# Performance work log

Measured on AMD Instinct MI355X. Metric: run time of the kernel, lower is better.

Reference implementation:

```python
import jax, jax.numpy as jnp
import numpy as np

N_NODES = 50000
N_EDGES = 800000
LATENT = 32
NODE_IN = 6
EDGE_IN = 3
STEPS = 10
OUT_DIM = 1
NEG_SLOPE = 0.01
LN_EPS = 1e-5


def _leaky(x):
    return jnp.where(x >= 0, x, NEG_SLOPE * x)


def _layernorm(x, scale, bias):
    mu = jnp.mean(x, axis=-1, keepdims=True)
    var = jnp.mean(jnp.square(x - mu), axis=-1, keepdims=True)
    return (x - mu) * jax.lax.rsqrt(var + LN_EPS) * scale + bias


def setup_inputs() -> dict:
    key = jax.random.key(0)
    ks = jax.random.split(key, 24)
    g = lambda i, shape, fan_in: (jax.random.normal(ks[i], shape, jnp.float32)
                                  / np.sqrt(fan_in)).astype(jnp.float32)
    return {
        "x": jax.random.normal(ks[0], (N_NODES, NODE_IN), jnp.float32),
        "edge_attr": jax.random.normal(ks[1], (N_EDGES, EDGE_IN), jnp.float32),
        "senders": jax.random.randint(ks[2], (N_EDGES,), 0, N_NODES, jnp.int32),
        "receivers": jax.random.randint(ks[3], (N_EDGES,), 0, N_NODES, jnp.int32),
        # input embedders (Linear + LeakyReLU)
        "node_enc_W": g(4, (NODE_IN, LATENT), NODE_IN),
        "node_enc_b": jnp.zeros((LATENT,), jnp.float32),
        "edge_enc_W": g(5, (EDGE_IN, LATENT), EDGE_IN),
        "edge_enc_b": jnp.zeros((LATENT,), jnp.float32),
        # per-step edge update: concat(e, x_src, x_dst) -> latent
        "edge_W": g(6, (STEPS, 3 * LATENT, LATENT), 3 * LATENT),
        "edge_b": jnp.zeros((STEPS, LATENT), jnp.float32),
        "edge_ln_scale": jnp.ones((STEPS, LATENT), jnp.float32),
        "edge_ln_bias": jnp.zeros((STEPS, LATENT), jnp.float32),
        # per-step node update: concat(x, agg) -> latent
        "node_W": g(7, (STEPS, 2 * LATENT, LATENT), 2 * LATENT),
        "node_b": jnp.zeros((STEPS, LATENT), jnp.float32),
        "node_ln_scale": jnp.ones((STEPS, LATENT), jnp.float32),
        "node_ln_bias": jnp.zeros((STEPS, LATENT), jnp.float32),
        # decoder
        "dec_W1": g(8, (LATENT, LATENT), LATENT),
        "dec_b1": jnp.zeros((LATENT,), jnp.float32),
        "dec_W2": g(9, (LATENT, OUT_DIM), LATENT),
        "dec_b2": jnp.zeros((OUT_DIM,), jnp.float32),
    }


def _forward(x, edge_attr, senders, receivers,
             node_enc_W, node_enc_b, edge_enc_W, edge_enc_b,
             edge_W, edge_b, edge_ln_scale, edge_ln_bias,
             node_W, node_b, node_ln_scale, node_ln_bias,
             dec_W1, dec_b1, dec_W2, dec_b2):
    n = x.shape[0]
    # encode raw features into latent space
    h = _leaky(x @ node_enc_W + node_enc_b)            # [N, L]
    e = _leaky(edge_attr @ edge_enc_W + edge_enc_b)    # [E, L]
    # receiver in-degree for scatter-mean (constant across steps)
    cnt = jax.ops.segment_sum(jnp.ones((e.shape[0],), e.dtype), receivers,
                              num_segments=n)
    inv_cnt = (1.0 / jnp.maximum(cnt, 1.0))[:, None]   # [N, 1]

    def step(carry, p):
        h, e = carry
        eW, eb, es, ebi, nW, nb, ns, nbi = p
        # edge update: MLP(concat(e, h_src, h_dst)) + inner LN + residual
        m = jnp.concatenate([e, h[senders], h[receivers]], axis=-1)  # [E, 3L]
        m = _layernorm(_leaky(m @ eW + eb), es, ebi)
        e = e + m
        # node update: scatter-mean over receivers, MLP + inner LN + residual
        agg = jax.ops.segment_sum(e, receivers, num_segments=n) * inv_cnt
        u = jnp.concatenate([h, agg], axis=-1)                       # [N, 2L]
        u = _layernorm(_leaky(u @ nW + nb), ns, nbi)
        h = h + u
        return (h, e), None

    (h, e), _ = jax.lax.scan(step, (h, e),
                             (edge_W, edge_b, edge_ln_scale, edge_ln_bias,
                              node_W, node_b, node_ln_scale, node_ln_bias))
    # decoder: Linear -> LeakyReLU -> Linear
    return _leaky(h @ dec_W1 + dec_b1) @ dec_W2 + dec_b2  # [N, 1]


def reference(x, edge_attr, senders, receivers,
              node_enc_W, node_enc_b, edge_enc_W, edge_enc_b,
              edge_W, edge_b, edge_ln_scale, edge_ln_bias,
              node_W, node_b, node_ln_scale, node_ln_bias,
              dec_W1, dec_b1, dec_W2, dec_b2):
    return _forward(x, edge_attr, senders, receivers,
                    node_enc_W, node_enc_b, edge_enc_W, edge_enc_b,
                    edge_W, edge_b, edge_ln_scale, edge_ln_bias,
                    node_W, node_b, node_ln_scale, node_ln_bias,
                    dec_W1, dec_b1, dec_W2, dec_b2)
```

## Files before the change

kernel.cpp:

```cpp
#include <hip/hip_runtime.h>
#include <hip/hip_bf16.h>

#define N_NODES 50000
#define N_EDGES 800000
#define LATENT 32
#define STEPS 10
#define NEG_SLOPE 0.01f
#define LN_EPS 1e-5f
#define SCAN_BLK 256
#define SCAN_NBLK ((N_NODES + SCAN_BLK - 1) / SCAN_BLK)
#define STG_STRIDE 36
#define NODES_PER_BLOCK 32
#define STEP_BLOCKS ((N_NODES + NODES_PER_BLOCK - 1) / NODES_PER_BLOCK)
#define WS_STRIDE 36

typedef __attribute__((ext_vector_type(8))) __bf16 bf16x8;
typedef __attribute__((ext_vector_type(4))) __bf16 bf16x4;
typedef __attribute__((ext_vector_type(4))) float f32x4;

__device__ __forceinline__ float leaky(float x) {
    return x >= 0.0f ? x : NEG_SLOPE * x;
}

__device__ __forceinline__ float4 f4fma(float a, float4 b, float4 c) {
    c.x += a * b.x; c.y += a * b.y; c.z += a * b.z; c.w += a * b.w;
    return c;
}

__device__ __forceinline__ bf16x4 pack4(float4 v) {
    bf16x4 o;
    o[0] = (__bf16)v.x; o[1] = (__bf16)v.y; o[2] = (__bf16)v.z; o[3] = (__bf16)v.w;
    return o;
}


__global__ void encode_nodes_kernel(const float* __restrict__ x,
                                    const float* __restrict__ W,
                                    const float* __restrict__ b,
                                    float* __restrict__ h,
                                    __bf16* __restrict__ hbf) {
    __shared__ __align__(16) float Ws[6 * 32];
    __shared__ __align__(16) float bs[32];
    int tid = threadIdx.x;
    if (tid < 192) Ws[tid] = W[tid];
    if (tid < 32) bs[tid] = b[tid];
    __syncthreads();
    int n = blockIdx.x * blockDim.x + tid;
    if (n >= N_NODES) return;
    float xv[6];
#pragma unroll
    for (int k = 0; k < 6; k++) xv[k] = x[(size_t)n * 6 + k];
    float4 acc[8];
#pragma unroll
    for (int q = 0; q < 8; q++) acc[q] = *(const float4*)&bs[q * 4];
#pragma unroll
    for (int k = 0; k < 6; k++) {
#pragma unroll
        for (int q = 0; q < 8; q++) {
            float4 w = *(const float4*)&Ws[k * 32 + q * 4];
            acc[q] = f4fma(xv[k], w, acc[q]);
        }
    }
#pragma unroll
    for (int q = 0; q < 8; q++) {
        float4 o = acc[q];
        o.x = leaky(o.x); o.y = leaky(o.y); o.z = leaky(o.z); o.w = leaky(o.w);
        *(float4*)&h[(size_t)n * 32 + q * 4] = o;
        *(bf16x4*)&hbf[(size_t)n * 32 + q * 4] = pack4(o);
    }
}


__global__ void count_kernel(const int* __restrict__ recv, int* __restrict__ cnt) {
    int i = blockIdx.x * blockDim.x + threadIdx.x;
    if (i < N_EDGES) atomicAdd(&cnt[recv[i]], 1);
}

__global__ void csr_reduce_kernel(const int* __restrict__ cnt, int* __restrict__ partial) {
    __shared__ int sdata[SCAN_BLK];
    int tid = threadIdx.x;
    int idx = blockIdx.x * SCAN_BLK + tid;
    sdata[tid] = (idx < N_NODES) ? cnt[idx] : 0;
    __syncthreads();
#pragma unroll
    for (int off = SCAN_BLK / 2; off > 0; off >>= 1) {
        if (tid < off) sdata[tid] += sdata[tid + off];
        __syncthreads();
    }
    if (tid == 0) partial[blockIdx.x] = sdata[0];
}

__global__ void csr_scan_partials_kernel(int* __restrict__ partial,
                                         int* __restrict__ row_start) {
    __shared__ int sdata[SCAN_BLK];
    int tid = threadIdx.x;
    int v = (tid < SCAN_NBLK) ? partial[tid] : 0;
    sdata[tid] = v;
    __syncthreads();
#pragma unroll
    for (int off = 1; off < SCAN_BLK; off <<= 1) {
        int t = (tid >= off) ? sdata[tid - off] : 0;
        __syncthreads();
        sdata[tid] += t;
        __syncthreads();
    }
    if (tid < SCAN_NBLK) partial[tid] = sdata[tid] - v;
    if (tid == SCAN_BLK - 1) row_start[N_NODES] = sdata[SCAN_BLK - 1];
}

__global__ void csr_apply_kernel(const int* __restrict__ cnt,
                                 const int* __restrict__ partial,
                                 int* __restrict__ row_start,
                                 int* __restrict__ cursor) {
    __shared__ int sdata[SCAN_BLK];
    int tid = threadIdx.x;
    int idx = blockIdx.x * SCAN_BLK + tid;
    int v = (idx < N_NODES) ? cnt[idx] : 0;
    sdata[tid] = v;
    __syncthreads();
#pragma unroll
    for (int off = 1; off < SCAN_BLK; off <<= 1) {
        int t = (tid >= off) ? sdata[tid - off] : 0;
        __syncthreads();
        sdata[tid] += t;
        __syncthreads();
    }
    if (idx < N_NODES) {
        int out = partial[blockIdx.x] + sdata[tid] - v;
        row_start[idx] = out;
        cursor[idx] = out;
    }
}

__global__ void scatter_encode_kernel(const float* __restrict__ ea,
                                      const int* __restrict__ senders,
                                      const int* __restrict__ receivers,
                                      int* __restrict__ cursor,
                                      const float* __restrict__ W,
                                      const float* __restrict__ b,
                                      __bf16* __restrict__ e,
                                      unsigned int* __restrict__ sr_p) {
    __shared__ __align__(16) float Ws[3 * 32];
    __shared__ __align__(16) float bs[32];
    int tid = threadIdx.x;
    if (tid < 96) Ws[tid] = W[tid];
    if (tid < 32) bs[tid] = b[tid];
    __syncthreads();
    int i = blockIdx.x * blockDim.x + tid;
    if (i >= N_EDGES) return;
    int s = senders[i];
    int r = receivers[i];
    float xv[3];
#pragma unroll
    for (int k = 0; k < 3; k++) xv[k] = ea[(size_t)i * 3 + k];
    int pos = atomicAdd(&cursor[r], 1);
    float4 acc[8];
#pragma unroll
    for (int q = 0; q < 8; q++) acc[q] = *(const float4*)&bs[q * 4];
#pragma unroll
    for (int k = 0; k < 3; k++) {
#pragma unroll
        for (int q = 0; q < 8; q++) {
            float4 w = *(const float4*)&Ws[k * 32 + q * 4];
            acc[q] = f4fma(xv[k], w, acc[q]);
        }
    }
    __bf16* er = e + (size_t)pos * 32;
#pragma unroll
    for (int q = 0; q < 4; q++) {
        float4 lo = acc[2 * q], hi = acc[2 * q + 1];
        bf16x8 v;
        v[0] = (__bf16)leaky(lo.x); v[1] = (__bf16)leaky(lo.y);
        v[2] = (__bf16)leaky(lo.z); v[3] = (__bf16)leaky(lo.w);
        v[4] = (__bf16)leaky(hi.x); v[5] = (__bf16)leaky(hi.y);
        v[6] = (__bf16)leaky(hi.z); v[7] = (__bf16)leaky(hi.w);
        *(bf16x8*)(er + q * 8) = v;
    }
    sr_p[pos] = (unsigned int)s | ((unsigned int)r << 16);
}


__global__ __launch_bounds__(256) void fused_step_kernel(
    __bf16* __restrict__ e,
    const __bf16* __restrict__ hbf_in,
    __bf16* __restrict__ hbf_out,
    const float* __restrict__ h_in,
    float* __restrict__ h_out,
    const unsigned int* __restrict__ srp,
    const int* __restrict__ row_start,
    const float* __restrict__ eW,
    const float* __restrict__ eb,
    const float* __restrict__ els,
    const float* __restrict__ elb,
    const float* __restrict__ nW,
    const float* __restrict__ nb,
    const float* __restrict__ nls,
    const float* __restrict__ nlb) {
    __shared__ __align__(16) float stg[4][16 * STG_STRIDE];
    __shared__ __align__(16) float Ws[64 * WS_STRIDE];
    __shared__ __align__(16) float prm[96];

    int tid = threadIdx.x;
    const int wave = tid >> 6;
    const int lane = tid & 63;
    const int n_ = lane & 15;
    const int quad = lane >> 4;
    const int rr = lane >> 2;
    const int jj = lane & 3;

    {
        const float4* Wg = (const float4*)nW;
#pragma unroll
        for (int r = 0; r < 2; r++) {
            int i4 = tid + r * 256;
            float4 val = Wg[i4];
            *(float4*)&Ws[(i4 >> 3) * WS_STRIDE + (i4 & 7) * 4] = val;
        }
        if (tid < 32) {
            prm[tid] = nb[tid];
            prm[32 + tid] = nls[tid];
            prm[64 + tid] = nlb[tid];
        }
    }

    bf16x8 bfr[3][2];
#pragma unroll
    for (int kc = 0; kc < 3; kc++)
#pragma unroll
        for (int oh = 0; oh < 2; oh++) {
            bf16x8 f;
#pragma unroll
            for (int j = 0; j < 8; j++)
                f[j] = (__bf16)eW[(kc * 32 + quad * 8 + j) * 32 + oh * 16 + n_];
            bfr[kc][oh] = f;
        }
    float bia0 = eb[n_], bia1 = eb[16 + n_];
    float lns8[8], lnb8[8];
    {
        f32x4 sa = *(const f32x4*)&els[jj * 8];
        f32x4 sb = *(const f32x4*)&els[jj * 8 + 4];
        f32x4 ba = *(const f32x4*)&elb[jj * 8];
        f32x4 bb = *(const f32x4*)&elb[jj * 8 + 4];
#pragma unroll
        for (int i = 0; i < 4; i++) {
            lns8[i] = sa[i]; lns8[4 + i] = sb[i];
            lnb8[i] = ba[i]; lnb8[4 + i] = bb[i];
        }
    }

    const int n0 = blockIdx.x * NODES_PER_BLOCK;
    const int nn = min(NODES_PER_BLOCK, N_NODES - n0);
    const int beg = row_start[n0];
    const int end = row_start[n0 + nn];
    const int nt = (end - beg + 15) >> 4;
    float* mystg = stg[wave];

    unsigned int sr_n2 = 0;
    bf16x8 aE{}, aS{}, aR{}, old{};
    if (wave < nt) {
        int jb = beg + wave * 16;
        int ja = min(jb + n_, N_EDGES - 1);
        unsigned int sr_c = srp[ja];
        aE  = *(const bf16x8*)&e[(size_t)ja * 32 + quad * 8];
        aS  = *(const bf16x8*)&hbf_in[(size_t)(sr_c & 0xFFFFu) * 32 + quad * 8];
        aR  = *(const bf16x8*)&hbf_in[(size_t)(sr_c >> 16) * 32 + quad * 8];
        old = *(const bf16x8*)&e[(size_t)min(jb + rr, N_EDGES - 1) * 32 + jj * 8];
        if (wave + 4 < nt)
            sr_n2 = srp[min(beg + (wave + 4) * 16 + n_, N_EDGES - 1)];
    }
    for (int t = wave; t < nt; t += 4) {
        int e0 = beg + t * 16;

        f32x4 acc[2] = {{0.f, 0.f, 0.f, 0.f}, {0.f, 0.f, 0.f, 0.f}};
#pragma unroll
        for (int oh = 0; oh < 2; oh++) {
            acc[oh] = __builtin_amdgcn_mfma_f32_16x16x32_bf16(aE, bfr[0][oh], acc[oh], 0, 0, 0);
            acc[oh] = __builtin_amdgcn_mfma_f32_16x16x32_bf16(aS, bfr[1][oh], acc[oh], 0, 0, 0);
            acc[oh] = __builtin_amdgcn_mfma_f32_16x16x32_bf16(aR, bfr[2][oh], acc[oh], 0, 0, 0);
        }

        bf16x8 aE_n = aE, aS_n = aS, aR_n = aR, old_n = old;
        if (t + 4 < nt) {
            int jb = beg + (t + 4) * 16;
            int ja = min(jb + n_, N_EDGES - 1);
            aE_n  = *(const bf16x8*)&e[(size_t)ja * 32 + quad * 8];
            aS_n  = *(const bf16x8*)&hbf_in[(size_t)(sr_n2 & 0xFFFFu) * 32 + quad * 8];
            aR_n  = *(const bf16x8*)&hbf_in[(size_t)(sr_n2 >> 16) * 32 + quad * 8];
            old_n = *(const bf16x8*)&e[(size_t)min(jb + rr, N_EDGES - 1) * 32 + jj * 8];
            if (t + 8 < nt)
                sr_n2 = srp[min(beg + (t + 8) * 16 + n_, N_EDGES - 1)];
        }

#pragma unroll
        for (int oh = 0; oh < 2; oh++)
#pragma unroll
            for (int g = 0; g < 4; g++)
                mystg[(quad * 4 + g) * STG_STRIDE + oh * 16 + n_] =
                    leaky(acc[oh][g] + (oh ? bia1 : bia0));
        __builtin_amdgcn_wave_barrier();

        f32x4 va = *(const f32x4*)&mystg[rr * STG_STRIDE + jj * 8];
        f32x4 vb = *(const f32x4*)&mystg[rr * STG_STRIDE + jj * 8 + 4];
        float s1 = va[0] + va[1] + va[2] + va[3] + vb[0] + vb[1] + vb[2] + vb[3];
        float s2 = va[0]*va[0] + va[1]*va[1] + va[2]*va[2] + va[3]*va[3]
                 + vb[0]*vb[0] + vb[1]*vb[1] + vb[2]*vb[2] + vb[3]*vb[3];
        s1 += __shfl_xor(s1, 1);  s2 += __shfl_xor(s2, 1);
        s1 += __shfl_xor(s1, 2);  s2 += __shfl_xor(s2, 2);
        float mu = s1 * (1.0f / 32.0f);
        float var = s2 * (1.0f / 32.0f) - mu * mu;
        float inv = rsqrtf(fmaxf(var, 0.0f) + LN_EPS);

        float v[8] = {va[0], va[1], va[2], va[3], vb[0], vb[1], vb[2], vb[3]};
        bf16x8 outp;
#pragma unroll
        for (int i = 0; i < 8; i++)
            outp[i] = (__bf16)((float)old[i] + (v[i] - mu) * inv * lns8[i] + lnb8[i]);
        if (e0 + rr < end)
            *(bf16x8*)&e[(size_t)(e0 + rr) * 32 + jj * 8] = outp;
        __builtin_amdgcn_wave_barrier();

        aE = aE_n; aS = aS_n; aR = aR_n; old = old_n;
    }

    __syncthreads();

    const int nl = tid >> 3;
    const int oc = tid & 7;
    const bool act = nl < nn;
    const int n = n0 + nl;
    float hv4[4] = {0.f, 0.f, 0.f, 0.f};
    float ag4[4] = {0.f, 0.f, 0.f, 0.f};
    if (act) {
        int bn = row_start[n], en = row_start[n + 1];
        float s4[4] = {0.f, 0.f, 0.f, 0.f};
        int j = bn;
        for (; j + 3 < en; j += 4) {
            bf16x4 v0 = *(const bf16x4*)&e[(size_t)j * 32 + oc * 4];
            bf16x4 v1 = *(const bf16x4*)&e[(size_t)(j + 1) * 32 + oc * 4];
            bf16x4 v2 = *(const bf16x4*)&e[(size_t)(j + 2) * 32 + oc * 4];
            bf16x4 v3 = *(const bf16x4*)&e[(size_t)(j + 3) * 32 + oc * 4];
#pragma unroll
            for (int k = 0; k < 4; k++)
                s4[k] += (float)v0[k] + (float)v1[k] + (float)v2[k] + (float)v3[k];
        }
        for (; j < en; j++) {
            bf16x4 v = *(const bf16x4*)&e[(size_t)j * 32 + oc * 4];
#pragma unroll
            for (int k = 0; k < 4; k++) s4[k] += (float)v[k];
        }
        float ic = 1.0f / fmaxf((float)(en - bn), 1.0f);
        float4 hvv = *(const float4*)&h_in[(size_t)n * 32 + oc * 4];
        hv4[0] = hvv.x; hv4[1] = hvv.y; hv4[2] = hvv.z; hv4[3] = hvv.w;
#pragma unroll
        for (int k = 0; k < 4; k++) ag4[k] = s4[k] * ic;
    }

    float4 acc[8];
#pragma unroll
    for (int q = 0; q < 8; q++) acc[q] = {0.f, 0.f, 0.f, 0.f};
#pragma unroll
    for (int kk = 0; kk < 4; kk++) {
        int kh = oc * 4 + kk;
        int ka = 32 + oc * 4 + kk;
#pragma unroll
        for (int q = 0; q < 8; q++) {
            acc[q] = f4fma(hv4[kk], *(const float4*)&Ws[kh * WS_STRIDE + q * 4], acc[q]);
            acc[q] = f4fma(ag4[kk], *(const float4*)&Ws[ka * WS_STRIDE + q * 4], acc[q]);
        }
    }
#pragma unroll
    for (int msk = 1; msk <= 4; msk <<= 1) {
#pragma unroll
        for (int q = 0; q < 8; q++) {
            acc[q].x += __shfl_xor(acc[q].x, msk);
            acc[q].y += __shfl_xor(acc[q].y, msk);
            acc[q].z += __shfl_xor(acc[q].z, msk);
            acc[q].w += __shfl_xor(acc[q].w, msk);
        }
    }

    if (act) {
        float s1 = 0.f, s2 = 0.f;
        float m_own[4];
#pragma unroll
        for (int q = 0; q < 8; q++) {
            float mq[4] = {leaky(acc[q].x + prm[q * 4 + 0]),
                           leaky(acc[q].y + prm[q * 4 + 1]),
                           leaky(acc[q].z + prm[q * 4 + 2]),
                           leaky(acc[q].w + prm[q * 4 + 3])};
#pragma unroll
            for (int k = 0; k < 4; k++) { s1 += mq[k]; s2 += mq[k] * mq[k]; }
            if (q == oc) {
#pragma unroll
                for (int k = 0; k < 4; k++) m_own[k] = mq[k];
            }
        }
        float mu = s1 * (1.0f / 32.0f);
        float var = s2 * (1.0f / 32.0f) - mu * mu;
        float inv = rsqrtf(fmaxf(var, 0.0f) + LN_EPS);
        float res[4];
#pragma unroll
        for (int k = 0; k < 4; k++)
            res[k] = hv4[k] + (m_own[k] - mu) * inv * prm[32 + oc * 4 + k] + prm[64 + oc * 4 + k];
        float4 r0 = {res[0], res[1], res[2], res[3]};
        *(float4*)&h_out[(size_t)n * 32 + oc * 4] = r0;
        *(bf16x4*)&hbf_out[(size_t)n * 32 + oc * 4] = pack4(r0);
    }
}


__global__ void decoder_kernel(const float* __restrict__ h,
                               const float* __restrict__ W1,
                               const float* __restrict__ b1,
                               const float* __restrict__ W2,
                               const float* __restrict__ b2,
                               float* __restrict__ out) {
    __shared__ __align__(16) float W1s[32 * 32];
    __shared__ __align__(16) float prm[65];
    int tid = threadIdx.x;
    {
        const float4* Wg = (const float4*)W1;
        float4* Wl = (float4*)W1s;
        Wl[tid] = Wg[tid];
        if (tid < 32) { prm[tid] = b1[tid]; prm[32 + tid] = W2[tid]; }
        if (tid == 0) prm[64] = b2[0];
    }
    __syncthreads();
    int n = blockIdx.x * blockDim.x + tid;
    if (n >= N_NODES) return;
    float hv[32];
#pragma unroll
    for (int q = 0; q < 8; q++) {
        float4 v = *(const float4*)&h[(size_t)n * 32 + q * 4];
        hv[q * 4 + 0] = v.x; hv[q * 4 + 1] = v.y; hv[q * 4 + 2] = v.z; hv[q * 4 + 3] = v.w;
    }
    float4 acc[8];
#pragma unroll
    for (int q = 0; q < 8; q++) acc[q] = *(const float4*)&prm[q * 4];
#pragma unroll
    for (int k = 0; k < 32; k++) {
#pragma unroll
        for (int q = 0; q < 8; q++) {
            float4 w = *(const float4*)&W1s[k * 32 + q * 4];
            acc[q] = f4fma(hv[k], w, acc[q]);
        }
    }
    float o = prm[64];
#pragma unroll
    for (int q = 0; q < 8; q++) {
        o += leaky(acc[q].x) * prm[32 + q * 4 + 0];
        o += leaky(acc[q].y) * prm[32 + q * 4 + 1];
        o += leaky(acc[q].z) * prm[32 + q * 4 + 2];
        o += leaky(acc[q].w) * prm[32 + q * 4 + 3];
    }
    out[n] = o;
}


extern "C" void kernel_launch(void* const* d_in, const int* in_sizes, int n_in,
                              void* d_out, int out_size, void* d_ws, size_t ws_size,
                              hipStream_t stream) {
    const float* x          = (const float*)d_in[0];
    const float* edge_attr  = (const float*)d_in[1];
    const int*   senders    = (const int*)d_in[2];
    const int*   receivers  = (const int*)d_in[3];
    const float* node_enc_W = (const float*)d_in[4];
    const float* node_enc_b = (const float*)d_in[5];
    const float* edge_enc_W = (const float*)d_in[6];
    const float* edge_enc_b = (const float*)d_in[7];
    const float* edge_W     = (const float*)d_in[8];
    const float* edge_b     = (const float*)d_in[9];
    const float* edge_ln_s  = (const float*)d_in[10];
    const float* edge_ln_b  = (const float*)d_in[11];
    const float* node_W     = (const float*)d_in[12];
    const float* node_b     = (const float*)d_in[13];
    const float* node_ln_s  = (const float*)d_in[14];
    const float* node_ln_b  = (const float*)d_in[15];
    const float* dec_W1     = (const float*)d_in[16];
    const float* dec_b1     = (const float*)d_in[17];
    const float* dec_W2     = (const float*)d_in[18];
    const float* dec_b2     = (const float*)d_in[19];
    float* out = (float*)d_out;

    char* ws = (char*)d_ws;
    size_t off = 0;
    auto alloc = [&](size_t bytes) -> void* {
        void* p = ws + off;
        off = (off + bytes + 255) & ~(size_t)255;
        return p;
    };
    float*        h0        = (float*)alloc((size_t)N_NODES * 32 * 4);
    float*        h1        = (float*)alloc((size_t)N_NODES * 32 * 4);
    __bf16*       hbf0      = (__bf16*)alloc((size_t)N_NODES * 32 * 2);
    __bf16*       hbf1      = (__bf16*)alloc((size_t)N_NODES * 32 * 2);
    __bf16*       e         = (__bf16*)alloc((size_t)N_EDGES * 32 * 2);
    int*          cnt       = (int*)alloc((size_t)N_NODES * 4);
    int*          row_start = (int*)alloc((size_t)(N_NODES + 1) * 4);
    int*          cursor    = (int*)alloc((size_t)N_NODES * 4);
    unsigned int* sr_p      = (unsigned int*)alloc((size_t)N_EDGES * 4);
    int*          partial   = (int*)alloc((size_t)SCAN_BLK * 4);
    (void)ws_size; (void)in_sizes; (void)n_in; (void)out_size;

    hipMemsetAsync(cnt, 0, (size_t)N_NODES * 4, stream);
    encode_nodes_kernel<<<(N_NODES + 255) / 256, 256, 0, stream>>>(x, node_enc_W, node_enc_b, h0, hbf0);
    count_kernel<<<(N_EDGES + 255) / 256, 256, 0, stream>>>(receivers, cnt);
    csr_reduce_kernel<<<SCAN_NBLK, SCAN_BLK, 0, stream>>>(cnt, partial);
    csr_scan_partials_kernel<<<1, SCAN_BLK, 0, stream>>>(partial, row_start);
    csr_apply_kernel<<<SCAN_NBLK, SCAN_BLK, 0, stream>>>(cnt, partial, row_start, cursor);
    scatter_encode_kernel<<<(N_EDGES + 255) / 256, 256, 0, stream>>>(
        edge_attr, senders, receivers, cursor, edge_enc_W, edge_enc_b, e, sr_p);

    float*  hbufs[2]  = {h0, h1};
    __bf16* hbbufs[2] = {hbf0, hbf1};
    for (int s = 0; s < STEPS; s++) {
        int in = s & 1, outb = 1 - in;
        fused_step_kernel<<<STEP_BLOCKS, 256, 0, stream>>>(
            e, hbbufs[in], hbbufs[outb], hbufs[in], hbufs[outb],
            sr_p, row_start,
            edge_W + (size_t)s * 96 * 32, edge_b + s * 32,
            edge_ln_s + s * 32, edge_ln_b + s * 32,
            node_W + (size_t)s * 64 * 32, node_b + s * 32,
            node_ln_s + s * 32, node_ln_b + s * 32);
    }
    decoder_kernel<<<(N_NODES + 255) / 256, 256, 0, stream>>>(h0, dec_W1, dec_b1, dec_W2, dec_b2, out);
}
```

Measured before the change: 714.9 us.

## Deepen edge-tile prefetch to two tiles, swizzle node weights, unroll aggregation

After: 663.7 us. 1.08x faster.

```diff
diff --git a/kernel.cpp b/kernel.cpp
--- a/kernel.cpp
+++ b/kernel.cpp
@@ -12,7 +12,6 @@
 #define STG_STRIDE 36
 #define NODES_PER_BLOCK 32
 #define STEP_BLOCKS ((N_NODES + NODES_PER_BLOCK - 1) / NODES_PER_BLOCK)
-#define WS_STRIDE 36
 
 typedef __attribute__((ext_vector_type(8))) __bf16 bf16x8;
 typedef __attribute__((ext_vector_type(4))) __bf16 bf16x4;
@@ -180,7 +179,7 @@
 }
 
 
-__global__ __launch_bounds__(256) void fused_step_kernel(
+__global__ __launch_bounds__(256, 3) void fused_step_kernel(
     __bf16* __restrict__ e,
     const __bf16* __restrict__ hbf_in,
     __bf16* __restrict__ hbf_out,
@@ -197,7 +196,7 @@
     const float* __restrict__ nls,
     const float* __restrict__ nlb) {
     __shared__ __align__(16) float stg[4][16 * STG_STRIDE];
-    __shared__ __align__(16) float Ws[64 * WS_STRIDE];
+    __shared__ __align__(16) float Ws[64 * 32];
     __shared__ __align__(16) float prm[96];
 
     int tid = threadIdx.x;
@@ -213,8 +212,9 @@
 #pragma unroll
         for (int r = 0; r < 2; r++) {
             int i4 = tid + r * 256;
-            float4 val = Wg[i4];
-            *(float4*)&Ws[(i4 >> 3) * WS_STRIDE + (i4 & 7) * 4] = val;
+            int row = i4 >> 3, q = i4 & 7;
+            int p = q ^ ((row >> 2) & 7);
+            *(float4*)&Ws[row * 32 + p * 4] = Wg[i4];
         }
         if (tid < 32) {
             prm[tid] = nb[tid];
@@ -255,41 +255,52 @@
     const int nt = (end - beg + 15) >> 4;
     float* mystg = stg[wave];
 
-    unsigned int sr_n2 = 0;
-    bf16x8 aE{}, aS{}, aR{}, old{};
+    unsigned int srA = 0;
+    bf16x8 aE0{}, aS0{}, aR0{}, old0{};
+    bf16x8 aE1{}, aS1{}, aR1{}, old1{};
     if (wave < nt) {
         int jb = beg + wave * 16;
         int ja = min(jb + n_, N_EDGES - 1);
-        unsigned int sr_c = srp[ja];
-        aE  = *(const bf16x8*)&e[(size_t)ja * 32 + quad * 8];
-        aS  = *(const bf16x8*)&hbf_in[(size_t)(sr_c & 0xFFFFu) * 32 + quad * 8];
-        aR  = *(const bf16x8*)&hbf_in[(size_t)(sr_c >> 16) * 32 + quad * 8];
-        old = *(const bf16x8*)&e[(size_t)min(jb + rr, N_EDGES - 1) * 32 + jj * 8];
-        if (wave + 4 < nt)
-            sr_n2 = srp[min(beg + (wave + 4) * 16 + n_, N_EDGES - 1)];
-    }
+        unsigned int sr = srp[ja];
+        aE0  = *(const bf16x8*)&e[(size_t)ja * 32 + quad * 8];
+        aS0  = *(const bf16x8*)&hbf_in[(size_t)(sr & 0xFFFFu) * 32 + quad * 8];
+        aR0  = *(const bf16x8*)&hbf_in[(size_t)(sr >> 16) * 32 + quad * 8];
+        old0 = *(const bf16x8*)&e[(size_t)min(jb + rr, N_EDGES - 1) * 32 + jj * 8];
+    }
+    if (wave + 4 < nt) {
+        int jb = beg + (wave + 4) * 16;
+        int ja = min(jb + n_, N_EDGES - 1);
+        unsigned int sr = srp[ja];
+        aE1  = *(const bf16x8*)&e[(size_t)ja * 32 + quad * 8];
+        aS1  = *(const bf16x8*)&hbf_in[(size_t)(sr & 0xFFFFu) * 32 + quad * 8];
+        aR1  = *(const bf16x8*)&hbf_in[(size_t)(sr >> 16) * 32 + quad * 8];
+        old1 = *(const bf16x8*)&e[(size_t)min(jb + rr, N_EDGES - 1) * 32 + jj * 8];
+    }
+    if (wave + 8 < nt)
+        srA = srp[min(beg + (wave + 8) * 16 + n_, N_EDGES - 1)];
+
     for (int t = wave; t < nt; t += 4) {
         int e0 = beg + t * 16;
 
         f32x4 acc[2] = {{0.f, 0.f, 0.f, 0.f}, {0.f, 0.f, 0.f, 0.f}};
 #pragma unroll
         for (int oh = 0; oh < 2; oh++) {
-            acc[oh] = __builtin_amdgcn_mfma_f32_16x16x32_bf16(aE, bfr[0][oh], acc[oh], 0, 0, 0);
-            acc[oh] = __builtin_amdgcn_mfma_f32_16x16x32_bf16(aS, bfr[1][oh], acc[oh], 0, 0, 0);
-            acc[oh] = __builtin_amdgcn_mfma_f32_16x16x32_bf16(aR, bfr[2][oh], acc[oh], 0, 0, 0);
-        }
-
-        bf16x8 aE_n = aE, aS_n = aS, aR_n = aR, old_n = old;
-        if (t + 4 < nt) {
-            int jb = beg + (t + 4) * 16;
+            acc[oh] = __builtin_amdgcn_mfma_f32_16x16x32_bf16(aE0, bfr[0][oh], acc[oh], 0, 0, 0);
+            acc[oh] = __builtin_amdgcn_mfma_f32_16x16x32_bf16(aS0, bfr[1][oh], acc[oh], 0, 0, 0);
+            acc[oh] = __builtin_amdgcn_mfma_f32_16x16x32_bf16(aR0, bfr[2][oh], acc[oh], 0, 0, 0);
+        }
+
+        bf16x8 aE2 = aE0, aS2 = aS0, aR2 = aR0, old2 = old0;
+        if (t + 8 < nt) {
+            int jb = beg + (t + 8) * 16;
             int ja = min(jb + n_, N_EDGES - 1);
-            aE_n  = *(const bf16x8*)&e[(size_t)ja * 32 + quad * 8];
-            aS_n  = *(const bf16x8*)&hbf_in[(size_t)(sr_n2 & 0xFFFFu) * 32 + quad * 8];
-            aR_n  = *(const bf16x8*)&hbf_in[(size_t)(sr_n2 >> 16) * 32 + quad * 8];
-            old_n = *(const bf16x8*)&e[(size_t)min(jb + rr, N_EDGES - 1) * 32 + jj * 8];
-            if (t + 8 < nt)
-                sr_n2 = srp[min(beg + (t + 8) * 16 + n_, N_EDGES - 1)];
-        }
+            aE2  = *(const bf16x8*)&e[(size_t)ja * 32 + quad * 8];
+            aS2  = *(const bf16x8*)&hbf_in[(size_t)(srA & 0xFFFFu) * 32 + quad * 8];
+            aR2  = *(const bf16x8*)&hbf_in[(size_t)(srA >> 16) * 32 + quad * 8];
+            old2 = *(const bf16x8*)&e[(size_t)min(jb + rr, N_EDGES - 1) * 32 + jj * 8];
+        }
+        if (t + 12 < nt)
+            srA = srp[min(beg + (t + 12) * 16 + n_, N_EDGES - 1)];
 
 #pragma unroll
         for (int oh = 0; oh < 2; oh++)
@@ -314,12 +325,13 @@
         bf16x8 outp;
 #pragma unroll
         for (int i = 0; i < 8; i++)
-            outp[i] = (__bf16)((float)old[i] + (v[i] - mu) * inv * lns8[i] + lnb8[i]);
+            outp[i] = (__bf16)((float)old0[i] + (v[i] - mu) * inv * lns8[i] + lnb8[i]);
         if (e0 + rr < end)
             *(bf16x8*)&e[(size_t)(e0 + rr) * 32 + jj * 8] = outp;
         __builtin_amdgcn_wave_barrier();
 
-        aE = aE_n; aS = aS_n; aR = aR_n; old = old_n;
+        aE0 = aE1; aS0 = aS1; aR0 = aR1; old0 = old1;
+        aE1 = aE2; aS1 = aS2; aR1 = aR2; old1 = old2;
     }
 
     __syncthreads();
@@ -334,14 +346,19 @@
         int bn = row_start[n], en = row_start[n + 1];
         float s4[4] = {0.f, 0.f, 0.f, 0.f};
         int j = bn;
-        for (; j + 3 < en; j += 4) {
-            bf16x4 v0 = *(const bf16x4*)&e[(size_t)j * 32 + oc * 4];
+        for (; j + 7 < en; j += 8) {
+            bf16x4 v0 = *(const bf16x4*)&e[(size_t)(j + 0) * 32 + oc * 4];
             bf16x4 v1 = *(const bf16x4*)&e[(size_t)(j + 1) * 32 + oc * 4];
             bf16x4 v2 = *(const bf16x4*)&e[(size_t)(j + 2) * 32 + oc * 4];
             bf16x4 v3 = *(const bf16x4*)&e[(size_t)(j + 3) * 32 + oc * 4];
+            bf16x4 v4 = *(const bf16x4*)&e[(size_t)(j + 4) * 32 + oc * 4];
+            bf16x4 v5 = *(const bf16x4*)&e[(size_t)(j + 5) * 32 + oc * 4];
+            bf16x4 v6 = *(const bf16x4*)&e[(size_t)(j + 6) * 32 + oc * 4];
+            bf16x4 v7 = *(const bf16x4*)&e[(size_t)(j + 7) * 32 + oc * 4];
 #pragma unroll
             for (int k = 0; k < 4; k++)
-                s4[k] += (float)v0[k] + (float)v1[k] + (float)v2[k] + (float)v3[k];
+                s4[k] += ((float)v0[k] + (float)v1[k]) + ((float)v2[k] + (float)v3[k])
+                       + ((float)v4[k] + (float)v5[k]) + ((float)v6[k] + (float)v7[k]);
         }
         for (; j < en; j++) {
             bf16x4 v = *(const bf16x4*)&e[(size_t)j * 32 + oc * 4];
@@ -355,27 +372,29 @@
         for (int k = 0; k < 4; k++) ag4[k] = s4[k] * ic;
     }
 
-    float4 acc[8];
-#pragma unroll
-    for (int q = 0; q < 8; q++) acc[q] = {0.f, 0.f, 0.f, 0.f};
+    float4 accn[8];
+#pragma unroll
+    for (int q = 0; q < 8; q++) accn[q] = {0.f, 0.f, 0.f, 0.f};
 #pragma unroll
     for (int kk = 0; kk < 4; kk++) {
         int kh = oc * 4 + kk;
-        int ka = 32 + oc * 4 + kk;
+        const float* rH = &Ws[kh * 32];
+        const float* rA = &Ws[(32 + kh) * 32];
 #pragma unroll
         for (int q = 0; q < 8; q++) {
-            acc[q] = f4fma(hv4[kk], *(const float4*)&Ws[kh * WS_STRIDE + q * 4], acc[q]);
-            acc[q] = f4fma(ag4[kk], *(const float4*)&Ws[ka * WS_STRIDE + q * 4], acc[q]);
+            int p = (q ^ oc) * 4;
+            accn[q] = f4fma(hv4[kk], *(const float4*)&rH[p], accn[q]);
+            accn[q] = f4fma(ag4[kk], *(const float4*)&rA[p], accn[q]);
         }
     }
 #pragma unroll
     for (int msk = 1; msk <= 4; msk <<= 1) {
 #pragma unroll
         for (int q = 0; q < 8; q++) {
-            acc[q].x += __shfl_xor(acc[q].x, msk);
-            acc[q].y += __shfl_xor(acc[q].y, msk);
-            acc[q].z += __shfl_xor(acc[q].z, msk);
-            acc[q].w += __shfl_xor(acc[q].w, msk);
+            accn[q].x += __shfl_xor(accn[q].x, msk);
+            accn[q].y += __shfl_xor(accn[q].y, msk);
+            accn[q].z += __shfl_xor(accn[q].z, msk);
+            accn[q].w += __shfl_xor(accn[q].w, msk);
         }
     }
 
@@ -384,10 +403,10 @@
         float m_own[4];
 #pragma unroll
         for (int q = 0; q < 8; q++) {
-            float mq[4] = {leaky(acc[q].x + prm[q * 4 + 0]),
-                           leaky(acc[q].y + prm[q * 4 + 1]),
-                           leaky(acc[q].z + prm[q * 4 + 2]),
-                           leaky(acc[q].w + prm[q * 4 + 3])};
+            float mq[4] = {leaky(accn[q].x + prm[q * 4 + 0]),
+                           leaky(accn[q].y + prm[q * 4 + 1]),
+                           leaky(accn[q].z + prm[q * 4 + 2]),
+                           leaky(accn[q].w + prm[q * 4 + 3])};
 #pragma unroll
             for (int k = 0; k < 4; k++) { s1 += mq[k]; s2 += mq[k] * mq[k]; }
             if (q == oc) {
```
